# Optimization experiments

Hardware: AMD Instinct MI355X
Metric: run time of the kernel (lower is better)

## Reference

```python
import jax, jax.numpy as jnp
import numpy as np

N_USER = 1_000_000
N_ITEM = 100_000
E = 16          # embedding_size
O = 16          # out_size per head
H = 4           # head_num
HID = 32        # hidden_size
B = 8192        # batch
S = 200         # sample_num
L = 50          # history length
NSUPP = 50_000  # supp_user_num


def _xavier(key, shape):
    fan_in, fan_out = shape[-2], shape[-1]
    std = np.sqrt(2.0 / (fan_in + fan_out))
    return (jax.random.normal(key, shape) * std).astype(jnp.float32)


def setup_inputs() -> dict:
    key = jax.random.key(0)
    ks = jax.random.split(key, 16)
    uid = jax.random.randint(ks[0], (B,), 0, N_USER)
    iid = jax.random.randint(ks[1], (B,), 0, N_ITEM)
    return {
        "user_embedding": _xavier(ks[2], (N_USER, E)),
        "item_embedding": _xavier(ks[3], (N_ITEM, E)),
        "wq": _xavier(ks[4], (H, E, O)),   # per-head Wq (no bias)
        "wk": _xavier(ks[5], (H, E, O)),
        "wv": _xavier(ks[6], (H, O, O)),
        "w_out": _xavier(ks[7], (H * O, O)),
        "l1_w": _xavier(ks[8], (3 * E, HID)),
        "l1_b": jnp.full((HID,), 0.1, jnp.float32),
        "l2_w": _xavier(ks[9], (HID, HID // 2)),
        "l2_b": jnp.full((HID // 2,), 0.1, jnp.float32),
        "l3_w": _xavier(ks[10], (HID // 2, 1)),
        "l3_b": jnp.full((1,), 0.1, jnp.float32),
        "user_bias": jnp.zeros((N_USER, 1), jnp.float32),
        "item_bias": jnp.zeros((N_ITEM, 1), jnp.float32),
        "x": jnp.stack([uid, iid], axis=1),                          # [B,2]
        "history": jax.random.randint(ks[11], (B, L), 0, N_ITEM),    # [B,L]
        "history_len": jax.random.randint(ks[12], (B,), 1, L + 1),   # [B] >=1
        "supp_users": jax.random.randint(ks[13], (NSUPP,), 0, N_USER),
        "sample_index": jax.random.randint(ks[14], (H, B, S), 0, NSUPP),
    }


def reference(user_embedding, item_embedding, wq, wk, wv, w_out,
              l1_w, l1_b, l2_w, l2_b, l3_w, l3_b, user_bias, item_bias,
              x, history, history_len, supp_users, sample_index):
    user_id = x[:, 0]
    item_id = x[:, 1]

    # user init embedding = mean-by-len of full (unmasked) history, as in source
    hist_emb = item_embedding[history]                                # [B,L,E]
    user_init = hist_emb.sum(axis=1) / history_len[:, None].astype(jnp.float32)  # [B,E]

    # per-head GAT over sampled support users (all heads vectorized)
    nb = user_embedding[supp_users[sample_index]]                     # [H,B,S,E]
    q = jnp.einsum('be,heo->hbo', user_init, wq)                      # [H,B,O]
    k = jnp.einsum('hbse,heo->hbso', nb, wk)                          # [H,B,S,O]
    attn = jax.nn.softmax(jnp.einsum('hbo,hbso->hbs', q, k), axis=-1)
    ctx = jnp.einsum('hbs,hbso->hbo', attn, k)                        # [H,B,O]
    gat = jnp.einsum('hbo,hop->hbp', ctx, wv)                         # [H,B,O]
    gat = jnp.transpose(gat, (1, 0, 2)).reshape(B, H * O)             # concat heads

    user_emb = gat @ w_out                                            # [B,O]
    item_emb = item_embedding[item_id]                                # [B,E]
    interaction = user_emb * item_emb
    ratings = interaction.sum(axis=1)

    h = jnp.concatenate([user_emb, item_emb, interaction], axis=1)    # [B,3E]
    x1 = jnp.tanh(h @ l1_w + l1_b)
    x2 = jnp.tanh(x1 @ l2_w + l2_b)
    x3 = (x2 @ l3_w + l3_b).reshape(-1)

    ub = user_bias[user_id, 0]
    ib = item_bias[item_id, 0]
    return (ratings + x3) / 2.0 + ub + ib
```

## Files before the change

### kernel.cpp

```cpp
#include <hip/hip_runtime.h>
#include <math.h>

#define N_USERS 1000000
#define N_ITEMS 100000
#define EMB 16
#define OUTD 16
#define NH 4
#define HID 32
#define BB 8192
#define SS 200
#define LL 50
#define NSUPP 50000

typedef float v4f __attribute__((ext_vector_type(4)));

__global__ __launch_bounds__(256) void k_supp_kernel(
    const float* __restrict__ user_emb,
    const int*   __restrict__ supp_users,
    const float* __restrict__ wk,
    float*       __restrict__ Ksupp)
{
    __shared__ float s_wk[NH * EMB * OUTD];
    __shared__ float s_u[16][EMB];
    int t = threadIdx.x;
    for (int i = t; i < NH * EMB * OUTD; i += 256) s_wk[i] = wk[i];
    int n0 = blockIdx.x * 16;
    {
        int ul = t >> 4, e = t & 15;
        int row = supp_users[n0 + ul];
        s_u[ul][e] = user_emb[(size_t)row * EMB + e];
    }
    __syncthreads();
    int h   = t >> 6;
    int sub = (t >> 4) & 3;
    int o   = t & 15;
#pragma unroll
    for (int r = 0; r < 4; ++r) {
        int ul = sub + 4 * r;
        float acc = 0.f;
#pragma unroll
        for (int e = 0; e < EMB; ++e)
            acc += s_u[ul][e] * s_wk[(h * EMB + e) * OUTD + o];
        Ksupp[((size_t)h * NSUPP + n0 + ul) * OUTD + o] = acc;
    }
}

__global__ __launch_bounds__(256) void user_init_q_kernel(
    const float* __restrict__ item_emb,
    const int*   __restrict__ history,
    const int*   __restrict__ history_len,
    const float* __restrict__ wq,
    float*       __restrict__ qbuf)
{
    __shared__ float s_ui[4][EMB];
    __shared__ float s_wq[NH * EMB * OUTD];
    int t = threadIdx.x;
    for (int i = t; i < NH * EMB * OUTD; i += 256) s_wq[i] = wq[i];

    int g    = t >> 6;
    int lane = t & 63;
    int l4   = lane >> 4;
    int e    = lane & 15;
    int b    = blockIdx.x * 4 + g;

    float sum = 0.f;
    for (int l = l4; l < LL; l += 4) {
        int it = __builtin_nontemporal_load(history + (size_t)b * LL + l);
        sum += item_emb[(size_t)it * EMB + e];
    }
    sum += __shfl_xor(sum, 16);
    sum += __shfl_xor(sum, 32);
    if (lane < EMB) s_ui[g][lane] = sum / (float)history_len[b];
    __syncthreads();

    int h  = (t >> 4) & 3;
    int o  = t & 15;
    float acc = 0.f;
#pragma unroll
    for (int ee = 0; ee < EMB; ++ee)
        acc += s_ui[g][ee] * s_wq[(h * EMB + ee) * OUTD + o];
    qbuf[((size_t)b * NH + h) * OUTD + o] = acc;
}

__global__ __launch_bounds__(256, 4) void attn_kernel(
    const float* __restrict__ Ksupp,
    const float* __restrict__ qbuf,
    const int*   __restrict__ sample_index,
    const float* __restrict__ wv,
    float*       __restrict__ gat)
{
    int blk   = blockIdx.x;
    int h     = (blk & 7) >> 1;
    int btile = ((blk >> 3) << 1) | (blk & 1);
    int wave  = threadIdx.x >> 6;
    int lane  = threadIdx.x & 63;
    int b     = btile * 4 + wave;
    int g     = lane >> 2;
    int qt    = lane & 3;

    const int* si = sample_index + ((size_t)h * BB + b) * SS;
    int pre0 = __builtin_nontemporal_load(si + lane);
    int pre1 = __builtin_nontemporal_load(si + lane + 64);
    int pre2 = __builtin_nontemporal_load(si + lane + 128);
    int pre3 = (lane < 8) ? __builtin_nontemporal_load(si + lane + 192) : 0;

    v4f qv = __builtin_nontemporal_load(
        (const v4f*)(qbuf + ((size_t)b * NH + h) * OUTD) + qt);

    const float* Kh = Ksupp + (size_t)h * NSUPP * OUTD;

    int idx[13];
#pragma unroll
    for (int r = 0; r < 13; ++r) {
        int pre = (r < 4) ? pre0 : (r < 8) ? pre1 : (r < 12) ? pre2 : pre3;
        idx[r] = __shfl(pre, (r & 3) * 16 + g, 64);
    }

    v4f kq[13];
#pragma unroll
    for (int r = 0; r < 13; ++r)
        kq[r] = *(const v4f*)(Kh + (size_t)idx[r] * OUTD + qt * 4);

    float d[13];
#pragma unroll
    for (int r = 0; r < 13; ++r) {
        float p = kq[r].x * qv.x + kq[r].y * qv.y + kq[r].z * qv.z + kq[r].w * qv.w;
        p += __shfl_xor(p, 1);
        p += __shfl_xor(p, 2);
        d[r] = p;
    }
    if (g >= 8) d[12] = -3.0e38f;

    float m = d[0];
#pragma unroll
    for (int r = 1; r < 13; ++r) m = fmaxf(m, d[r]);
#pragma unroll
    for (int off = 4; off < 64; off <<= 1) m = fmaxf(m, __shfl_xor(m, off));

    float l = 0.f;
    v4f c = {0.f, 0.f, 0.f, 0.f};
#pragma unroll
    for (int r = 0; r < 13; ++r) {
        float w = __expf(d[r] - m);
        l += w;
        c += w * kq[r];
    }
#pragma unroll
    for (int off = 4; off < 64; off <<= 1) {
        l   += __shfl_xor(l, off);
        c.x += __shfl_xor(c.x, off);
        c.y += __shfl_xor(c.y, off);
        c.z += __shfl_xor(c.z, off);
        c.w += __shfl_xor(c.w, off);
    }
    float inv = 1.f / l;

    float part = c.x * wv[((size_t)h * OUTD + qt * 4 + 0) * OUTD + g]
               + c.y * wv[((size_t)h * OUTD + qt * 4 + 1) * OUTD + g]
               + c.z * wv[((size_t)h * OUTD + qt * 4 + 2) * OUTD + g]
               + c.w * wv[((size_t)h * OUTD + qt * 4 + 3) * OUTD + g];
    part += __shfl_xor(part, 1);
    part += __shfl_xor(part, 2);
    if (qt == 0)
        gat[(size_t)b * (NH * OUTD) + h * OUTD + g] = part * inv;
}

__global__ __launch_bounds__(256) void epilogue_kernel(
    const float* __restrict__ gat,
    const float* __restrict__ item_emb,
    const float* __restrict__ w_out,
    const float* __restrict__ l1_w, const float* __restrict__ l1_b,
    const float* __restrict__ l2_w, const float* __restrict__ l2_b,
    const float* __restrict__ l3_w, const float* __restrict__ l3_b,
    const float* __restrict__ user_bias, const float* __restrict__ item_bias,
    const int*   __restrict__ x,
    float*       __restrict__ out)
{
    int t    = threadIdx.x;
    int g    = t >> 6;
    int lane = t & 63;
    int b    = blockIdx.x * 4 + g;

    __shared__ float s_gat[4][NH * OUTD];
    __shared__ float s_ue[4][OUTD];
    __shared__ float s_ie[4][EMB];
    __shared__ float s_x1[4][HID];
    __shared__ float s_x2[4][HID / 2];

    int uid = x[(size_t)b * 2 + 0];
    int iid = x[(size_t)b * 2 + 1];

    s_gat[g][lane] = gat[(size_t)b * (NH * OUTD) + lane];
    if (lane < EMB) s_ie[g][lane] = item_emb[(size_t)iid * EMB + lane];
    __syncthreads();

    if (lane < OUTD) {
        float acc = 0.f;
#pragma unroll
        for (int j = 0; j < NH * OUTD; ++j) acc += s_gat[g][j] * w_out[j * OUTD + lane];
        s_ue[g][lane] = acc;
    }
    __syncthreads();

    if (lane < HID) {
        float acc = l1_b[lane];
#pragma unroll
        for (int i = 0; i < EMB; ++i) {
            float ue = s_ue[g][i], ie = s_ie[g][i];
            acc += ue * l1_w[i * HID + lane]
                 + ie * l1_w[(EMB + i) * HID + lane]
                 + ue * ie * l1_w[(2 * EMB + i) * HID + lane];
        }
        s_x1[g][lane] = tanhf(acc);
    }
    __syncthreads();

    if (lane < HID / 2) {
        float acc = l2_b[lane];
#pragma unroll
        for (int j = 0; j < HID; ++j) acc += s_x1[g][j] * l2_w[j * (HID / 2) + lane];
        s_x2[g][lane] = tanhf(acc);
    }
    __syncthreads();

    if (lane == 0) {
        float x3 = l3_b[0];
#pragma unroll
        for (int j = 0; j < HID / 2; ++j) x3 += s_x2[g][j] * l3_w[j];
        float ratings = 0.f;
#pragma unroll
        for (int o = 0; o < OUTD; ++o) ratings += s_ue[g][o] * s_ie[g][o];
        out[b] = 0.5f * (ratings + x3) + user_bias[uid] + item_bias[iid];
    }
}

extern "C" void kernel_launch(void* const* d_in, const int* in_sizes, int n_in,
                              void* d_out, int out_size, void* d_ws, size_t ws_size,
                              hipStream_t stream) {
    const float* user_embedding = (const float*)d_in[0];
    const float* item_embedding = (const float*)d_in[1];
    const float* wq             = (const float*)d_in[2];
    const float* wk             = (const float*)d_in[3];
    const float* wv             = (const float*)d_in[4];
    const float* w_out          = (const float*)d_in[5];
    const float* l1_w           = (const float*)d_in[6];
    const float* l1_b           = (const float*)d_in[7];
    const float* l2_w           = (const float*)d_in[8];
    const float* l2_b           = (const float*)d_in[9];
    const float* l3_w           = (const float*)d_in[10];
    const float* l3_b           = (const float*)d_in[11];
    const float* user_bias      = (const float*)d_in[12];
    const float* item_bias      = (const float*)d_in[13];
    const int*   x              = (const int*)d_in[14];
    const int*   history        = (const int*)d_in[15];
    const int*   history_len    = (const int*)d_in[16];
    const int*   supp_users     = (const int*)d_in[17];
    const int*   sample_index   = (const int*)d_in[18];
    float* out = (float*)d_out;

    char* ws = (char*)d_ws;
    float* Ksupp = (float*)ws;
    ws += (size_t)NH * NSUPP * OUTD * sizeof(float);
    float* qbuf  = (float*)ws;
    ws += (size_t)BB * NH * OUTD * sizeof(float);
    float* gat   = (float*)ws;

    k_supp_kernel<<<NSUPP / 16, 256, 0, stream>>>(user_embedding, supp_users, wk, Ksupp);
    user_init_q_kernel<<<BB / 4, 256, 0, stream>>>(item_embedding, history, history_len, wq, qbuf);
    attn_kernel<<<NH * BB / 4, 256, 0, stream>>>(Ksupp, qbuf, sample_index, wv, gat);
    epilogue_kernel<<<BB / 4, 256, 0, stream>>>(
        gat, item_embedding, w_out, l1_w, l1_b, l2_w, l2_b, l3_w, l3_b,
        user_bias, item_bias, x, out);
}
```

Before: 214.0 us.

## Merge setup kernels, load sample indices directly, use DPP for intra-row reductions

Fuses the support-key projection and user-init query kernels into one launch that branches on block index, removing a kernel launch and letting the two independent stages overlap. In the attention kernel, each lane now loads its sample indices directly (clamped, so some lanes issue redundant loads) instead of loading once and redistributing with shuffles. Lane reductions within a row now use DPP quad-permute and row-shift modifiers in place of shuffles for the small strides, with shuffles kept only for the cross-row strides of 16 and 32.

```diff
diff --git a/kernel.cpp b/kernel.cpp
--- a/kernel.cpp
+++ b/kernel.cpp
@@ -11,75 +11,77 @@
 #define SS 200
 #define LL 50
 #define NSUPP 50000
+#define KS_BLOCKS (NSUPP / 16)
 
 typedef float v4f __attribute__((ext_vector_type(4)));
 
-__global__ __launch_bounds__(256) void k_supp_kernel(
+#define DPPF(x, ctrl) \
+    __int_as_float(__builtin_amdgcn_update_dpp(0, __float_as_int(x), ctrl, 0xF, 0xF, true))
+
+__global__ __launch_bounds__(256) void setup_kernel(
     const float* __restrict__ user_emb,
     const int*   __restrict__ supp_users,
     const float* __restrict__ wk,
-    float*       __restrict__ Ksupp)
-{
-    __shared__ float s_wk[NH * EMB * OUTD];
-    __shared__ float s_u[16][EMB];
-    int t = threadIdx.x;
-    for (int i = t; i < NH * EMB * OUTD; i += 256) s_wk[i] = wk[i];
-    int n0 = blockIdx.x * 16;
-    {
-        int ul = t >> 4, e = t & 15;
-        int row = supp_users[n0 + ul];
-        s_u[ul][e] = user_emb[(size_t)row * EMB + e];
-    }
-    __syncthreads();
-    int h   = t >> 6;
-    int sub = (t >> 4) & 3;
-    int o   = t & 15;
-#pragma unroll
-    for (int r = 0; r < 4; ++r) {
-        int ul = sub + 4 * r;
-        float acc = 0.f;
-#pragma unroll
-        for (int e = 0; e < EMB; ++e)
-            acc += s_u[ul][e] * s_wk[(h * EMB + e) * OUTD + o];
-        Ksupp[((size_t)h * NSUPP + n0 + ul) * OUTD + o] = acc;
-    }
-}
-
-__global__ __launch_bounds__(256) void user_init_q_kernel(
+    float*       __restrict__ Ksupp,
     const float* __restrict__ item_emb,
     const int*   __restrict__ history,
     const int*   __restrict__ history_len,
     const float* __restrict__ wq,
     float*       __restrict__ qbuf)
 {
-    __shared__ float s_ui[4][EMB];
-    __shared__ float s_wq[NH * EMB * OUTD];
     int t = threadIdx.x;
-    for (int i = t; i < NH * EMB * OUTD; i += 256) s_wq[i] = wq[i];
-
-    int g    = t >> 6;
-    int lane = t & 63;
-    int l4   = lane >> 4;
-    int e    = lane & 15;
-    int b    = blockIdx.x * 4 + g;
-
-    float sum = 0.f;
-    for (int l = l4; l < LL; l += 4) {
-        int it = __builtin_nontemporal_load(history + (size_t)b * LL + l);
-        sum += item_emb[(size_t)it * EMB + e];
-    }
-    sum += __shfl_xor(sum, 16);
-    sum += __shfl_xor(sum, 32);
-    if (lane < EMB) s_ui[g][lane] = sum / (float)history_len[b];
-    __syncthreads();
-
-    int h  = (t >> 4) & 3;
-    int o  = t & 15;
-    float acc = 0.f;
-#pragma unroll
-    for (int ee = 0; ee < EMB; ++ee)
-        acc += s_ui[g][ee] * s_wq[(h * EMB + ee) * OUTD + o];
-    qbuf[((size_t)b * NH + h) * OUTD + o] = acc;
+    if (blockIdx.x < KS_BLOCKS) {
+        __shared__ float s_wk[NH * EMB * OUTD];
+        __shared__ float s_u[16][EMB];
+        for (int i = t; i < NH * EMB * OUTD; i += 256) s_wk[i] = wk[i];
+        int n0 = blockIdx.x * 16;
+        {
+            int ul = t >> 4, e = t & 15;
+            int row = supp_users[n0 + ul];
+            s_u[ul][e] = user_emb[(size_t)row * EMB + e];
+        }
+        __syncthreads();
+        int h   = t >> 6;
+        int sub = (t >> 4) & 3;
+        int o   = t & 15;
+#pragma unroll
+        for (int r = 0; r < 4; ++r) {
+            int ul = sub + 4 * r;
+            float acc = 0.f;
+#pragma unroll
+            for (int e = 0; e < EMB; ++e)
+                acc += s_u[ul][e] * s_wk[(h * EMB + e) * OUTD + o];
+            Ksupp[((size_t)h * NSUPP + n0 + ul) * OUTD + o] = acc;
+        }
+    } else {
+        __shared__ float s_ui[4][EMB];
+        __shared__ float s_wq[NH * EMB * OUTD];
+        for (int i = t; i < NH * EMB * OUTD; i += 256) s_wq[i] = wq[i];
+
+        int g    = t >> 6;
+        int lane = t & 63;
+        int l4   = lane >> 4;
+        int e    = lane & 15;
+        int b    = (blockIdx.x - KS_BLOCKS) * 4 + g;
+
+        float sum = 0.f;
+        for (int l = l4; l < LL; l += 4) {
+            int it = __builtin_nontemporal_load(history + (size_t)b * LL + l);
+            sum += item_emb[(size_t)it * EMB + e];
+        }
+        sum += __shfl_xor(sum, 16);
+        sum += __shfl_xor(sum, 32);
+        if (lane < EMB) s_ui[g][lane] = sum / (float)history_len[b];
+        __syncthreads();
+
+        int h = (t >> 4) & 3;
+        int o = t & 15;
+        float acc = 0.f;
+#pragma unroll
+        for (int ee = 0; ee < EMB; ++ee)
+            acc += s_ui[g][ee] * s_wq[(h * EMB + ee) * OUTD + o];
+        qbuf[((size_t)b * NH + h) * OUTD + o] = acc;
+    }
 }
 
 __global__ __launch_bounds__(256, 4) void attn_kernel(
@@ -99,23 +101,19 @@
     int qt    = lane & 3;
 
     const int* si = sample_index + ((size_t)h * BB + b) * SS;
-    int pre0 = __builtin_nontemporal_load(si + lane);
-    int pre1 = __builtin_nontemporal_load(si + lane + 64);
-    int pre2 = __builtin_nontemporal_load(si + lane + 128);
-    int pre3 = (lane < 8) ? __builtin_nontemporal_load(si + lane + 192) : 0;
+    int idx[13];
+#pragma unroll
+    for (int r = 0; r < 13; ++r) {
+        int s = r * 16 + g;
+        if (s > SS - 1) s = SS - 1;
+        idx[r] = __builtin_nontemporal_load(si + s);
+    }
 
     v4f qv = __builtin_nontemporal_load(
         (const v4f*)(qbuf + ((size_t)b * NH + h) * OUTD) + qt);
 
     const float* Kh = Ksupp + (size_t)h * NSUPP * OUTD;
 
-    int idx[13];
-#pragma unroll
-    for (int r = 0; r < 13; ++r) {
-        int pre = (r < 4) ? pre0 : (r < 8) ? pre1 : (r < 12) ? pre2 : pre3;
-        idx[r] = __shfl(pre, (r & 3) * 16 + g, 64);
-    }
-
     v4f kq[13];
 #pragma unroll
     for (int r = 0; r < 13; ++r)
@@ -125,8 +123,8 @@
 #pragma unroll
     for (int r = 0; r < 13; ++r) {
         float p = kq[r].x * qv.x + kq[r].y * qv.y + kq[r].z * qv.z + kq[r].w * qv.w;
-        p += __shfl_xor(p, 1);
-        p += __shfl_xor(p, 2);
+        p += DPPF(p, 0xB1);
+        p += DPPF(p, 0x4E);
         d[r] = p;
     }
     if (g >= 8) d[12] = -3.0e38f;
@@ -134,8 +132,10 @@
     float m = d[0];
 #pragma unroll
     for (int r = 1; r < 13; ++r) m = fmaxf(m, d[r]);
-#pragma unroll
-    for (int off = 4; off < 64; off <<= 1) m = fmaxf(m, __shfl_xor(m, off));
+    m = fmaxf(m, DPPF(m, 0x124));
+    m = fmaxf(m, DPPF(m, 0x128));
+    m = fmaxf(m, __shfl_xor(m, 16));
+    m = fmaxf(m, __shfl_xor(m, 32));
 
     float l = 0.f;
     v4f c = {0.f, 0.f, 0.f, 0.f};
@@ -145,22 +145,24 @@
         l += w;
         c += w * kq[r];
     }
-#pragma unroll
-    for (int off = 4; off < 64; off <<= 1) {
-        l   += __shfl_xor(l, off);
-        c.x += __shfl_xor(c.x, off);
-        c.y += __shfl_xor(c.y, off);
-        c.z += __shfl_xor(c.z, off);
-        c.w += __shfl_xor(c.w, off);
-    }
+    l   += DPPF(l,   0x124); l   += DPPF(l,   0x128);
+    c.x += DPPF(c.x, 0x124); c.x += DPPF(c.x, 0x128);
+    c.y += DPPF(c.y, 0x124); c.y += DPPF(c.y, 0x128);
+    c.z += DPPF(c.z, 0x124); c.z += DPPF(c.z, 0x128);
+    c.w += DPPF(c.w, 0x124); c.w += DPPF(c.w, 0x128);
+    l   += __shfl_xor(l,   16); l   += __shfl_xor(l,   32);
+    c.x += __shfl_xor(c.x, 16); c.x += __shfl_xor(c.x, 32);
+    c.y += __shfl_xor(c.y, 16); c.y += __shfl_xor(c.y, 32);
+    c.z += __shfl_xor(c.z, 16); c.z += __shfl_xor(c.z, 32);
+    c.w += __shfl_xor(c.w, 16); c.w += __shfl_xor(c.w, 32);
     float inv = 1.f / l;
 
     float part = c.x * wv[((size_t)h * OUTD + qt * 4 + 0) * OUTD + g]
                + c.y * wv[((size_t)h * OUTD + qt * 4 + 1) * OUTD + g]
                + c.z * wv[((size_t)h * OUTD + qt * 4 + 2) * OUTD + g]
                + c.w * wv[((size_t)h * OUTD + qt * 4 + 3) * OUTD + g];
-    part += __shfl_xor(part, 1);
-    part += __shfl_xor(part, 2);
+    part += DPPF(part, 0xB1);
+    part += DPPF(part, 0x4E);
     if (qt == 0)
         gat[(size_t)b * (NH * OUTD) + h * OUTD + g] = part * inv;
 }
@@ -265,8 +267,9 @@
     ws += (size_t)BB * NH * OUTD * sizeof(float);
     float* gat   = (float*)ws;
 
-    k_supp_kernel<<<NSUPP / 16, 256, 0, stream>>>(user_embedding, supp_users, wk, Ksupp);
-    user_init_q_kernel<<<BB / 4, 256, 0, stream>>>(item_embedding, history, history_len, wq, qbuf);
+    setup_kernel<<<KS_BLOCKS + BB / 4, 256, 0, stream>>>(
+        user_embedding, supp_users, wk, Ksupp,
+        item_embedding, history, history_len, wq, qbuf);
     attn_kernel<<<NH * BB / 4, 256, 0, stream>>>(Ksupp, qbuf, sample_index, wv, gat);
     epilogue_kernel<<<BB / 4, 256, 0, stream>>>(
         gat, item_embedding, w_out, l1_w, l1_b, l2_w, l2_b, l3_w, l3_b,
```

Result: slower. 219.7 us (+2.7%).
